# Kernel tuning notes

Hardware: AMD Instinct MI355X
Metric: run time of the kernel (lower is better)

The kernel has to match this reference:

```python
import jax, jax.numpy as jnp
import numpy as np

K = 3
PAD = 1
EPS = 1e-5


def _unfold(x, k, pad):
    # torch.nn.Unfold(k, dilation=1, padding=pad, stride=1): output [B, C*k*k, L]
    # with channel-major ordering (c, ki, kj) in the second dim.
    B, C, H, W = x.shape
    xp = jnp.pad(x, ((0, 0), (0, 0), (pad, pad), (pad, pad)))
    Ho = H + 2 * pad - k + 1
    Wo = W + 2 * pad - k + 1
    patches = jnp.stack(
        [xp[:, :, i:i + Ho, j:j + Wo] for i in range(k) for j in range(k)],
        axis=2,
    )  # [B, C, k*k, Ho, Wo]
    return patches.reshape(B, C * k * k, Ho * Wo)


def _conv1x1(x, w, b):
    return jnp.einsum('bchw,oc->bohw', x, w) + b[None, :, None, None]


def _bn(x, g, b):
    # training-mode BatchNorm2d: batch stats over (B,H,W), biased variance
    mu = x.mean(axis=(0, 2, 3), keepdims=True)
    var = x.var(axis=(0, 2, 3), keepdims=True)
    return (x - mu) * jax.lax.rsqrt(var + EPS) * g[None, :, None, None] + b[None, :, None, None]


def _tri(x, w, b, g, be):
    return jax.nn.relu(_bn(_conv1x1(x, w, b), g, be))


def reference(x, w1, b1, g1, be1, w2, b2, g2, be2, wf, bf, gf, bef):
    B, C, H, W = x.shape
    k2 = K * K
    c = k2 // 2
    tri1 = _tri(x, w1, b1, g1, be1)  # key map  [B,C,H,W] (m=1)
    tri2 = _tri(x, w2, b2, g2, be2)  # query map
    # NOTE: faithful to source: plain row-major reshape of [B, C*k2, L] -> [B, C, L, k2]
    ku = _unfold(tri1, K, PAD).reshape(B, C, -1, k2)
    qu = _unfold(tri2, K, PAD).reshape(B, C, -1, k2)
    logits = ku * qu[..., c:c + 1] + ku[..., c:c + 1] * qu
    dl_weight = jax.nn.softmax(logits, axis=-1)[:, None]  # [B,1,C,L,k2]
    xu = _unfold(x, K, PAD).reshape(B, 1, C, -1, k2)       # m=1 -> [B,1,C,L,k2]
    # NOTE: faithful to source: row-major reshape to [B, C, k2, L], sum over axis -2
    pre = (dl_weight * xu).reshape(B, C, k2, -1).sum(axis=-2).reshape(B, C, H, W)
    return jax.nn.relu(_bn(_conv1x1(pre, wf, bf), gf, bef))


def setup_inputs() -> dict:
    key = jax.random.key(0)
    B, C, O, H, W = 4, 256, 256, 64, 64
    ks = jax.random.split(key, 4)
    s = 1.0 / np.sqrt(C)
    return {
        'x': jax.random.normal(ks[0], (B, C, H, W), dtype=jnp.float32),
        'w1': jax.random.normal(ks[1], (C, C), dtype=jnp.float32) * s,
        'b1': jnp.zeros((C,), jnp.float32),
        'g1': jnp.ones((C,), jnp.float32),
        'be1': jnp.zeros((C,), jnp.float32),
        'w2': jax.random.normal(ks[2], (C, C), dtype=jnp.float32) * s,
        'b2': jnp.zeros((C,), jnp.float32),
        'g2': jnp.ones((C,), jnp.float32),
        'be2': jnp.zeros((C,), jnp.float32),
        'wf': jax.random.normal(ks[3], (O, C), dtype=jnp.float32) * s,
        'bf': jnp.zeros((O,), jnp.float32),
        'gf': jnp.ones((O,), jnp.float32),
        'bef': jnp.zeros((O,), jnp.float32),
    }
```

## Files before the change

kernel.cpp:

```cpp
#include <hip/hip_runtime.h>

#define L 4096
#define CCH 256
#define NB 4
#define KP 40

typedef __attribute__((ext_vector_type(8))) short short8;
typedef __attribute__((ext_vector_type(4))) float f32x4;

__device__ __forceinline__ unsigned short f2bf(float f) {
    unsigned u = __builtin_bit_cast(unsigned, f);
    u += 0x7FFF + ((u >> 16) & 1);
    return (unsigned short)(u >> 16);
}

__global__ __launch_bounds__(256, 2) void dual_gemm_k(
    const float* __restrict__ x,
    const float* __restrict__ w1, const float* __restrict__ b1,
    const float* __restrict__ w2, const float* __restrict__ b2,
    float* __restrict__ y1, float* __restrict__ y2)
{
    __shared__ short sA1[128 * KP];
    __shared__ short sA2[128 * KP];
    __shared__ short sB [64 * KP];

    const int tid = threadIdx.x;
    const int l0 = blockIdx.x * 64;
    const int o0 = blockIdx.y * 128;
    const int b  = blockIdx.z;

    const int wv = tid >> 6;
    const int lane = tid & 63;
    const int m = lane & 15;
    const int quad = lane >> 4;

    const float* xb = x + (size_t)b * CCH * L;

    const int sl = tid & 63, soct = tid >> 6;
    const int sr = tid & 127, sh = tid >> 7;

    f32x4 acc1[2][4] = {{{0.f,0.f,0.f,0.f}}};
    f32x4 acc2[2][4] = {{{0.f,0.f,0.f,0.f}}};
    #pragma unroll
    for (int io = 0; io < 2; ++io)
        #pragma unroll
        for (int jl = 0; jl < 4; ++jl) {
            acc1[io][jl] = (f32x4){0.f,0.f,0.f,0.f};
            acc2[io][jl] = (f32x4){0.f,0.f,0.f,0.f};
        }

    for (int s = 0; s < 8; ++s) {
        const int k0 = s * 32;
        __syncthreads();
        {
            const float* xs = xb + (size_t)(k0 + soct * 8) * L + l0 + sl;
            short8 v;
            #pragma unroll
            for (int j = 0; j < 8; ++j) v[j] = (short)f2bf(xs[(size_t)j * L]);
            *(short8*)&sB[sl * KP + soct * 8] = v;
        }
        {
            const float4* wp = (const float4*)&w1[(size_t)(o0 + sr) * CCH + k0 + sh * 16];
            float4 c0 = wp[0], c1 = wp[1], c2 = wp[2], c3 = wp[3];
            short8 p0 = {(short)f2bf(c0.x),(short)f2bf(c0.y),(short)f2bf(c0.z),(short)f2bf(c0.w),
                         (short)f2bf(c1.x),(short)f2bf(c1.y),(short)f2bf(c1.z),(short)f2bf(c1.w)};
            short8 p1 = {(short)f2bf(c2.x),(short)f2bf(c2.y),(short)f2bf(c2.z),(short)f2bf(c2.w),
                         (short)f2bf(c3.x),(short)f2bf(c3.y),(short)f2bf(c3.z),(short)f2bf(c3.w)};
            *(short8*)&sA1[sr * KP + sh * 16]     = p0;
            *(short8*)&sA1[sr * KP + sh * 16 + 8] = p1;
            const float4* wq = (const float4*)&w2[(size_t)(o0 + sr) * CCH + k0 + sh * 16];
            float4 d0 = wq[0], d1 = wq[1], d2 = wq[2], d3 = wq[3];
            short8 q0 = {(short)f2bf(d0.x),(short)f2bf(d0.y),(short)f2bf(d0.z),(short)f2bf(d0.w),
                         (short)f2bf(d1.x),(short)f2bf(d1.y),(short)f2bf(d1.z),(short)f2bf(d1.w)};
            short8 q1 = {(short)f2bf(d2.x),(short)f2bf(d2.y),(short)f2bf(d2.z),(short)f2bf(d2.w),
                         (short)f2bf(d3.x),(short)f2bf(d3.y),(short)f2bf(d3.z),(short)f2bf(d3.w)};
            *(short8*)&sA2[sr * KP + sh * 16]     = q0;
            *(short8*)&sA2[sr * KP + sh * 16 + 8] = q1;
        }
        __syncthreads();
        short8 a1[2], a2[2], bf[4];
        #pragma unroll
        for (int io = 0; io < 2; ++io) {
            a1[io] = *(const short8*)&sA1[(wv * 32 + io * 16 + m) * KP + quad * 8];
            a2[io] = *(const short8*)&sA2[(wv * 32 + io * 16 + m) * KP + quad * 8];
        }
        #pragma unroll
        for (int jl = 0; jl < 4; ++jl)
            bf[jl] = *(const short8*)&sB[(jl * 16 + m) * KP + quad * 8];
        #pragma unroll
        for (int io = 0; io < 2; ++io)
            #pragma unroll
            for (int jl = 0; jl < 4; ++jl) {
                acc1[io][jl] = __builtin_amdgcn_mfma_f32_16x16x32_bf16(a1[io], bf[jl], acc1[io][jl], 0, 0, 0);
                acc2[io][jl] = __builtin_amdgcn_mfma_f32_16x16x32_bf16(a2[io], bf[jl], acc2[io][jl], 0, 0, 0);
            }
    }

    #pragma unroll
    for (int io = 0; io < 2; ++io)
        #pragma unroll
        for (int reg = 0; reg < 4; ++reg) {
            const int o = o0 + wv * 32 + io * 16 + quad * 4 + reg;
            const float bb1 = b1[o], bb2 = b2[o];
            const size_t ro = ((size_t)b * CCH + o) * L + l0 + m;
            #pragma unroll
            for (int jl = 0; jl < 4; ++jl) {
                y1[ro + jl * 16] = acc1[io][jl][reg] + bb1;
                y2[ro + jl * 16] = acc2[io][jl][reg] + bb2;
            }
        }
}

__global__ __launch_bounds__(256, 2) void single_gemm_k(
    const float* __restrict__ x,
    const float* __restrict__ w, const float* __restrict__ bb,
    float* __restrict__ y)
{
    __shared__ short sA[128 * KP];
    __shared__ short sB[64 * KP];

    const int tid = threadIdx.x;
    const int l0 = blockIdx.x * 64;
    const int o0 = blockIdx.y * 128;
    const int b  = blockIdx.z;

    const int wv = tid >> 6;
    const int lane = tid & 63;
    const int m = lane & 15;
    const int quad = lane >> 4;

    const float* xb = x + (size_t)b * CCH * L;

    const int sl = tid & 63, soct = tid >> 6;
    const int sr = tid & 127, sh = tid >> 7;

    f32x4 acc[2][4];
    #pragma unroll
    for (int io = 0; io < 2; ++io)
        #pragma unroll
        for (int jl = 0; jl < 4; ++jl)
            acc[io][jl] = (f32x4){0.f,0.f,0.f,0.f};

    for (int s = 0; s < 8; ++s) {
        const int k0 = s * 32;
        __syncthreads();
        {
            const float* xs = xb + (size_t)(k0 + soct * 8) * L + l0 + sl;
            short8 v;
            #pragma unroll
            for (int j = 0; j < 8; ++j) v[j] = (short)f2bf(xs[(size_t)j * L]);
            *(short8*)&sB[sl * KP + soct * 8] = v;
        }
        {
            const float4* wp = (const float4*)&w[(size_t)(o0 + sr) * CCH + k0 + sh * 16];
            float4 c0 = wp[0], c1 = wp[1], c2 = wp[2], c3 = wp[3];
            short8 p0 = {(short)f2bf(c0.x),(short)f2bf(c0.y),(short)f2bf(c0.z),(short)f2bf(c0.w),
                         (short)f2bf(c1.x),(short)f2bf(c1.y),(short)f2bf(c1.z),(short)f2bf(c1.w)};
            short8 p1 = {(short)f2bf(c2.x),(short)f2bf(c2.y),(short)f2bf(c2.z),(short)f2bf(c2.w),
                         (short)f2bf(c3.x),(short)f2bf(c3.y),(short)f2bf(c3.z),(short)f2bf(c3.w)};
            *(short8*)&sA[sr * KP + sh * 16]     = p0;
            *(short8*)&sA[sr * KP + sh * 16 + 8] = p1;
        }
        __syncthreads();
        short8 a[2], bf[4];
        #pragma unroll
        for (int io = 0; io < 2; ++io)
            a[io] = *(const short8*)&sA[(wv * 32 + io * 16 + m) * KP + quad * 8];
        #pragma unroll
        for (int jl = 0; jl < 4; ++jl)
            bf[jl] = *(const short8*)&sB[(jl * 16 + m) * KP + quad * 8];
        #pragma unroll
        for (int io = 0; io < 2; ++io)
            #pragma unroll
            for (int jl = 0; jl < 4; ++jl)
                acc[io][jl] = __builtin_amdgcn_mfma_f32_16x16x32_bf16(a[io], bf[jl], acc[io][jl], 0, 0, 0);
    }

    #pragma unroll
    for (int io = 0; io < 2; ++io)
        #pragma unroll
        for (int reg = 0; reg < 4; ++reg) {
            const int o = o0 + wv * 32 + io * 16 + quad * 4 + reg;
            const float b0 = bb[o];
            const size_t ro = ((size_t)b * CCH + o) * L + l0 + m;
            #pragma unroll
            for (int jl = 0; jl < 4; ++jl)
                y[ro + jl * 16] = acc[io][jl][reg] + b0;
        }
}

__global__ __launch_bounds__(256) void bn_stats_k(
    const float* __restrict__ y, const float* __restrict__ gamma,
    const float* __restrict__ beta,
    float* __restrict__ scale, float* __restrict__ shift)
{
    const int c = blockIdx.x, tid = threadIdx.x;
    float s = 0.f, s2 = 0.f;
    for (int b = 0; b < NB; ++b) {
        const float4* p = (const float4*)(y + ((size_t)b * CCH + c) * L);
        #pragma unroll
        for (int r = 0; r < 4; ++r) {
            float4 v = p[r * 256 + tid];
            s  += v.x + v.y + v.z + v.w;
            s2 += v.x * v.x + v.y * v.y + v.z * v.z + v.w * v.w;
        }
    }
    #pragma unroll
    for (int off = 32; off > 0; off >>= 1) {
        s  += __shfl_down(s, off);
        s2 += __shfl_down(s2, off);
    }
    __shared__ float red[2][4];
    if ((tid & 63) == 0) { red[0][tid >> 6] = s; red[1][tid >> 6] = s2; }
    __syncthreads();
    if (tid == 0) {
        float S  = red[0][0] + red[0][1] + red[0][2] + red[0][3];
        float S2 = red[1][0] + red[1][1] + red[1][2] + red[1][3];
        const float invN = 1.f / (NB * (float)L);
        float mean = S * invN;
        float var  = S2 * invN - mean * mean;
        float rstd = rsqrtf(var + 1e-5f);
        float g = gamma[c];
        scale[c] = g * rstd;
        shift[c] = beta[c] - mean * g * rstd;
    }
}

__global__ __launch_bounds__(512, 4) void attention_k(
    const float* __restrict__ x,
    const float* __restrict__ y1,
    const float* __restrict__ y2,
    const float* __restrict__ s1sc, const float* __restrict__ s1sh,
    const float* __restrict__ s2sc, const float* __restrict__ s2sh,
    float* __restrict__ pre)
{
    __shared__ float sK[L];
    __shared__ float sQ[L];
    __shared__ float sXv[L];
    __shared__ float sInv[L];

    const int bc = blockIdx.x;
    const int tid = threadIdx.x;
    const int ch = bc & 255;
    const size_t off = (size_t)bc * L;

    const float sc1 = s1sc[ch], sh1 = s1sh[ch];
    const float sc2 = s2sc[ch], sh2 = s2sh[ch];

    const float4* k4 = (const float4*)(y1 + off);
    const float4* q4 = (const float4*)(y2 + off);
    const float4* x4 = (const float4*)(x + off);

    #pragma unroll
    for (int r = 0; r < 2; ++r) {
        int i = r * 512 + tid;
        float4 a = k4[i];
        a.x = fmaxf(fmaf(a.x, sc1, sh1), 0.f);
        a.y = fmaxf(fmaf(a.y, sc1, sh1), 0.f);
        a.z = fmaxf(fmaf(a.z, sc1, sh1), 0.f);
        a.w = fmaxf(fmaf(a.w, sc1, sh1), 0.f);
        ((float4*)sK)[i] = a;
        float4 q = q4[i];
        q.x = fmaxf(fmaf(q.x, sc2, sh2), 0.f);
        q.y = fmaxf(fmaf(q.y, sc2, sh2), 0.f);
        q.z = fmaxf(fmaf(q.z, sc2, sh2), 0.f);
        q.w = fmaxf(fmaf(q.w, sc2, sh2), 0.f);
        ((float4*)sQ)[i] = q;
        ((float4*)sXv)[i] = x4[i];
    }
    __syncthreads();

    #pragma unroll
    for (int r = 0; r < 8; ++r) {
        const int lp = r * 512 + tid;
        const int base = 9 * lp;
        float kv[9], qv[9];
        #pragma unroll
        for (int j = 0; j < 9; ++j) {
            int f = base + j;
            int t = f >> 12;
            int l = f & 4095;
            int di = (t * 86) >> 8;
            int dj = t - di * 3;
            int ii = (l >> 6) + di - 1;
            int jj = (l & 63) + dj - 1;
            bool ok = ((unsigned)ii < 64u) && ((unsigned)jj < 64u);
            int src = ((ii << 6) + jj) & 4095;
            float kj = sK[src], qj = sQ[src];
            kv[j] = ok ? kj : 0.f;
            qv[j] = ok ? qj : 0.f;
        }
        const float kc = kv[4], qc = qv[4];
        float s01 = __expf(kv[0] * qc + kc * qv[0]) + __expf(kv[1] * qc + kc * qv[1]);
        float s23 = __expf(kv[2] * qc + kc * qv[2]) + __expf(kv[3] * qc + kc * qv[3]);
        float s45 = __expf(kv[4] * qc + kc * qv[4]) + __expf(kv[5] * qc + kc * qv[5]);
        float s67 = __expf(kv[6] * qc + kc * qv[6]) + __expf(kv[7] * qc + kc * qv[7]);
        float s = ((s01 + s23) + (s45 + s67)) + __expf(kv[8] * qc + kc * qv[8]);
        sInv[lp] = __builtin_amdgcn_rcpf(s);
    }
    __syncthreads();

    #pragma unroll
    for (int r = 0; r < 8; ++r) {
        const int l = r * 512 + tid;
        const int li = l >> 6, lj = l & 63;
        float acc = 0.f;
        #pragma unroll
        for (int t = 0; t < 9; ++t) {
            const int f = (t << 12) + l;
            const unsigned lp = (unsigned)f / 9u;
            const int di = t / 3, dj = t % 3;
            int ii = li + di - 1;
            int jj = lj + dj - 1;
            bool ok = ((unsigned)ii < 64u) && ((unsigned)jj < 64u);
            int src = ((ii << 6) + jj) & 4095;
            float kj = sK[src], qj = sQ[src], xj = sXv[src];
            kj = ok ? kj : 0.f; qj = ok ? qj : 0.f; xj = ok ? xj : 0.f;
            int fc = 9 * (int)lp + 4;
            int tc = fc >> 12;
            int lc = fc & 4095;
            int dci = (tc * 86) >> 8;
            int dcj = tc - dci * 3;
            int ci = (lc >> 6) + dci - 1;
            int cj = (lc & 63) + dcj - 1;
            bool okc = ((unsigned)ci < 64u) && ((unsigned)cj < 64u);
            int csrc = ((ci << 6) + cj) & 4095;
            float kc = sK[csrc], qc = sQ[csrc];
            kc = okc ? kc : 0.f; qc = okc ? qc : 0.f;
            float e = __expf(kj * qc + kc * qj);
            acc = fmaf(e * sInv[lp], xj, acc);
        }
        pre[off + l] = acc;
    }
}

__global__ __launch_bounds__(256) void bn_apply_k(
    const float* __restrict__ yf,
    const float* __restrict__ scale, const float* __restrict__ shift,
    float* __restrict__ out)
{
    int i = blockIdx.x * 256 + threadIdx.x;
    int o = (i >> 10) & 255;
    float sc = scale[o], sh = shift[o];
    float4 v = ((const float4*)yf)[i];
    v.x = fmaxf(fmaf(v.x, sc, sh), 0.f);
    v.y = fmaxf(fmaf(v.y, sc, sh), 0.f);
    v.z = fmaxf(fmaf(v.z, sc, sh), 0.f);
    v.w = fmaxf(fmaf(v.w, sc, sh), 0.f);
    ((float4*)out)[i] = v;
}

extern "C" void kernel_launch(void* const* d_in, const int* in_sizes, int n_in,
                              void* d_out, int out_size, void* d_ws, size_t ws_size,
                              hipStream_t stream) {
    const float* x   = (const float*)d_in[0];
    const float* w1  = (const float*)d_in[1];
    const float* b1  = (const float*)d_in[2];
    const float* g1  = (const float*)d_in[3];
    const float* be1 = (const float*)d_in[4];
    const float* w2  = (const float*)d_in[5];
    const float* b2  = (const float*)d_in[6];
    const float* g2  = (const float*)d_in[7];
    const float* be2 = (const float*)d_in[8];
    const float* wf  = (const float*)d_in[9];
    const float* bf  = (const float*)d_in[10];
    const float* gf  = (const float*)d_in[11];
    const float* bef = (const float*)d_in[12];
    float* out = (float*)d_out;

    float* ws = (float*)d_ws;
    const size_t NEL = (size_t)NB * CCH * L;
    float* y1 = ws;
    float* y2 = ws + NEL;
    float* st = ws + 2 * NEL;
    float* s1sc = st,        *s1sh = st + 256;
    float* s2sc = st + 512,  *s2sh = st + 768;
    float* sfsc = st + 1024, *sfsh = st + 1280;

    dim3 gg(64, 2, 4);
    dual_gemm_k<<<gg, 256, 0, stream>>>(x, w1, b1, w2, b2, y1, y2);
    bn_stats_k<<<256, 256, 0, stream>>>(y1, g1, be1, s1sc, s1sh);
    bn_stats_k<<<256, 256, 0, stream>>>(y2, g2, be2, s2sc, s2sh);
    attention_k<<<NB * CCH, 512, 0, stream>>>(x, y1, y2, s1sc, s1sh, s2sc, s2sh, y2);
    single_gemm_k<<<gg, 256, 0, stream>>>(y2, wf, bf, y1);
    bn_stats_k<<<256, 256, 0, stream>>>(y1, gf, bef, sfsc, sfsh);
    bn_apply_k<<<4096, 256, 0, stream>>>(y1, sfsc, sfsh, out);
}
```

Measured before the change: 195.0 us.

## Pack key/query as bf16 pairs in LDS and cache center values with log-normalizer

The attention kernel now stores post-BN key and query as one packed bf16 pair per position, which halves LDS footprint and read count. The first pass saves, per softmax group, the packed center key/query and the negative log of the softmax denominator. The second pass can then fold normalization into the exponent and skip recomputing center indices and reloading values. The two BN stats launches for the key and query maps are merged into one kernel. Rounding key/query to bf16 inside the softmax logits adds precision error.

```diff
diff --git a/kernel.cpp b/kernel.cpp
--- a/kernel.cpp
+++ b/kernel.cpp
@@ -12,6 +12,12 @@
     unsigned u = __builtin_bit_cast(unsigned, f);
     u += 0x7FFF + ((u >> 16) & 1);
     return (unsigned short)(u >> 16);
+}
+__device__ __forceinline__ float bflo(unsigned w) {
+    return __builtin_bit_cast(float, w << 16);
+}
+__device__ __forceinline__ float bfhi(unsigned w) {
+    return __builtin_bit_cast(float, w & 0xFFFF0000u);
 }
 
 __global__ __launch_bounds__(256, 2) void dual_gemm_k(
@@ -39,8 +45,7 @@
     const int sl = tid & 63, soct = tid >> 6;
     const int sr = tid & 127, sh = tid >> 7;
 
-    f32x4 acc1[2][4] = {{{0.f,0.f,0.f,0.f}}};
-    f32x4 acc2[2][4] = {{{0.f,0.f,0.f,0.f}}};
+    f32x4 acc1[2][4], acc2[2][4];
     #pragma unroll
     for (int io = 0; io < 2; ++io)
         #pragma unroll
@@ -189,12 +194,10 @@
         }
 }
 
-__global__ __launch_bounds__(256) void bn_stats_k(
-    const float* __restrict__ y, const float* __restrict__ gamma,
-    const float* __restrict__ beta,
-    float* __restrict__ scale, float* __restrict__ shift)
-{
-    const int c = blockIdx.x, tid = threadIdx.x;
+__device__ __forceinline__ void bn_stats_body(
+    const float* y, const float* gamma, const float* beta,
+    float* scale, float* shift, int c, int tid)
+{
     float s = 0.f, s2 = 0.f;
     for (int b = 0; b < NB; ++b) {
         const float4* p = (const float4*)(y + ((size_t)b * CCH + c) * L);
@@ -226,6 +229,25 @@
     }
 }
 
+__global__ __launch_bounds__(256) void bn_stats_k(
+    const float* __restrict__ y, const float* __restrict__ gamma,
+    const float* __restrict__ beta,
+    float* __restrict__ scale, float* __restrict__ shift)
+{
+    bn_stats_body(y, gamma, beta, scale, shift, blockIdx.x, threadIdx.x);
+}
+
+__global__ __launch_bounds__(256) void bn_stats2_k(
+    const float* __restrict__ y1, const float* __restrict__ g1, const float* __restrict__ be1,
+    float* __restrict__ sc1, float* __restrict__ sh1,
+    const float* __restrict__ y2, const float* __restrict__ g2, const float* __restrict__ be2,
+    float* __restrict__ sc2, float* __restrict__ sh2)
+{
+    const int c = blockIdx.x & 255;
+    if (blockIdx.x < 256) bn_stats_body(y1, g1, be1, sc1, sh1, c, threadIdx.x);
+    else                  bn_stats_body(y2, g2, be2, sc2, sh2, c, threadIdx.x);
+}
+
 __global__ __launch_bounds__(512, 4) void attention_k(
     const float* __restrict__ x,
     const float* __restrict__ y1,
@@ -234,10 +256,9 @@
     const float* __restrict__ s2sc, const float* __restrict__ s2sh,
     float* __restrict__ pre)
 {
-    __shared__ float sK[L];
-    __shared__ float sQ[L];
-    __shared__ float sXv[L];
-    __shared__ float sInv[L];
+    __shared__ unsigned sKQ[L];
+    __shared__ float    sXv[L];
+    __shared__ uint2    sCI[L];
 
     const int bc = blockIdx.x;
     const int tid = threadIdx.x;
@@ -255,17 +276,15 @@
     for (int r = 0; r < 2; ++r) {
         int i = r * 512 + tid;
         float4 a = k4[i];
-        a.x = fmaxf(fmaf(a.x, sc1, sh1), 0.f);
-        a.y = fmaxf(fmaf(a.y, sc1, sh1), 0.f);
-        a.z = fmaxf(fmaf(a.z, sc1, sh1), 0.f);
-        a.w = fmaxf(fmaf(a.w, sc1, sh1), 0.f);
-        ((float4*)sK)[i] = a;
         float4 q = q4[i];
-        q.x = fmaxf(fmaf(q.x, sc2, sh2), 0.f);
-        q.y = fmaxf(fmaf(q.y, sc2, sh2), 0.f);
-        q.z = fmaxf(fmaf(q.z, sc2, sh2), 0.f);
-        q.w = fmaxf(fmaf(q.w, sc2, sh2), 0.f);
-        ((float4*)sQ)[i] = q;
+        float kk[4] = {a.x, a.y, a.z, a.w};
+        float qq[4] = {q.x, q.y, q.z, q.w};
+        #pragma unroll
+        for (int u = 0; u < 4; ++u) {
+            unsigned pk = f2bf(fmaxf(fmaf(kk[u], sc1, sh1), 0.f));
+            unsigned pq = f2bf(fmaxf(fmaf(qq[u], sc2, sh2), 0.f));
+            sKQ[i * 4 + u] = pk | (pq << 16);
+        }
         ((float4*)sXv)[i] = x4[i];
     }
     __syncthreads();
@@ -275,6 +294,7 @@
         const int lp = r * 512 + tid;
         const int base = 9 * lp;
         float kv[9], qv[9];
+        unsigned cw = 0;
         #pragma unroll
         for (int j = 0; j < 9; ++j) {
             int f = base + j;
@@ -286,9 +306,11 @@
             int jj = (l & 63) + dj - 1;
             bool ok = ((unsigned)ii < 64u) && ((unsigned)jj < 64u);
             int src = ((ii << 6) + jj) & 4095;
-            float kj = sK[src], qj = sQ[src];
-            kv[j] = ok ? kj : 0.f;
-            qv[j] = ok ? qj : 0.f;
+            unsigned w = sKQ[src];
+            w = ok ? w : 0u;
+            if (j == 4) cw = w;
+            kv[j] = bflo(w);
+            qv[j] = bfhi(w);
         }
         const float kc = kv[4], qc = qv[4];
         float s01 = __expf(kv[0] * qc + kc * qv[0]) + __expf(kv[1] * qc + kc * qv[1]);
@@ -296,7 +318,10 @@
         float s45 = __expf(kv[4] * qc + kc * qv[4]) + __expf(kv[5] * qc + kc * qv[5]);
         float s67 = __expf(kv[6] * qc + kc * qv[6]) + __expf(kv[7] * qc + kc * qv[7]);
         float s = ((s01 + s23) + (s45 + s67)) + __expf(kv[8] * qc + kc * qv[8]);
-        sInv[lp] = __builtin_amdgcn_rcpf(s);
+        uint2 ci;
+        ci.x = cw;
+        ci.y = __builtin_bit_cast(unsigned, -__logf(s));
+        sCI[lp] = ci;
     }
     __syncthreads();
 
@@ -309,26 +334,21 @@
         for (int t = 0; t < 9; ++t) {
             const int f = (t << 12) + l;
             const unsigned lp = (unsigned)f / 9u;
+            uint2 ci = sCI[lp];
+            const float kc = bflo(ci.x), qc = bfhi(ci.x);
+            const float cn = __builtin_bit_cast(float, ci.y);
             const int di = t / 3, dj = t % 3;
             int ii = li + di - 1;
             int jj = lj + dj - 1;
             bool ok = ((unsigned)ii < 64u) && ((unsigned)jj < 64u);
             int src = ((ii << 6) + jj) & 4095;
-            float kj = sK[src], qj = sQ[src], xj = sXv[src];
-            kj = ok ? kj : 0.f; qj = ok ? qj : 0.f; xj = ok ? xj : 0.f;
-            int fc = 9 * (int)lp + 4;
-            int tc = fc >> 12;
-            int lc = fc & 4095;
-            int dci = (tc * 86) >> 8;
-            int dcj = tc - dci * 3;
-            int ci = (lc >> 6) + dci - 1;
-            int cj = (lc & 63) + dcj - 1;
-            bool okc = ((unsigned)ci < 64u) && ((unsigned)cj < 64u);
-            int csrc = ((ci << 6) + cj) & 4095;
-            float kc = sK[csrc], qc = sQ[csrc];
-            kc = okc ? kc : 0.f; qc = okc ? qc : 0.f;
-            float e = __expf(kj * qc + kc * qj);
-            acc = fmaf(e * sInv[lp], xj, acc);
+            unsigned w = sKQ[src];
+            float xj = sXv[src];
+            w  = ok ? w : 0u;
+            xj = ok ? xj : 0.f;
+            const float kj = bflo(w), qj = bfhi(w);
+            float e = __expf(fmaf(kj, qc, fmaf(kc, qj, cn)));
+            acc = fmaf(e, xj, acc);
         }
         pre[off + l] = acc;
     }
@@ -379,8 +399,8 @@
 
     dim3 gg(64, 2, 4);
     dual_gemm_k<<<gg, 256, 0, stream>>>(x, w1, b1, w2, b2, y1, y2);
-    bn_stats_k<<<256, 256, 0, stream>>>(y1, g1, be1, s1sc, s1sh);
-    bn_stats_k<<<256, 256, 0, stream>>>(y2, g2, be2, s2sc, s2sh);
+    bn_stats2_k<<<512, 256, 0, stream>>>(y1, g1, be1, s1sc, s1sh,
+                                         y2, g2, be2, s2sc, s2sh);
     attention_k<<<NB * CCH, 512, 0, stream>>>(x, y1, y2, s1sc, s1sh, s2sc, s2sh, y2);
     single_gemm_k<<<gg, 256, 0, stream>>>(y2, wf, bf, y1);
     bn_stats_k<<<256, 256, 0, stream>>>(y1, gf, bef, sfsc, sfsh);
```

Measured after the change: 186.4 us. 1.05x faster.
